# Kernel optimization log

Measured on AMD Instinct MI355X. Metric: run time of the kernel, lower is better.

Reference implementation:

```python
import jax, jax.numpy as jnp
import numpy as np

N_NODES = 100000
N_EDGES = 1600000
N_GRAPHS = 2000
IN_DIM = 37
HID = 128
OUT_CLS = 2


def _leconv(x, src, dst, w, W1, b1, W2, W3, b3):
    # PyG LEConv: out[i] = sum_j w_ij * (lin1(x)[i] - lin2(x)[j]) + lin3(x)[i]
    a = x @ W1 + b1          # [N, H]
    b = x @ W2               # [N, H] (lin2 has no bias)
    c = x @ W3 + b3          # [N, H]
    deg = jax.ops.segment_sum(w, dst, num_segments=N_NODES)              # [N]
    agg = jax.ops.segment_sum(w[:, None] * b[src], dst, num_segments=N_NODES)  # [N, H]
    return deg[:, None] * a - agg + c


def setup_inputs() -> dict:
    key = jax.random.key(0)
    ks = jax.random.split(key, 32)
    inp = {}
    inp["x"] = jax.random.normal(ks[0], (N_NODES, IN_DIM), dtype=jnp.float32)
    inp["edge_index"] = jax.random.randint(ks[1], (2, N_EDGES), 0, N_NODES, dtype=jnp.int64)
    inp["batch"] = jnp.sort(jax.random.randint(ks[2], (N_NODES,), 0, N_GRAPHS, dtype=jnp.int64))
    dims = [(IN_DIM, HID), (HID, HID), (HID, HID)]
    ki = 3
    for l, (di, do) in enumerate(dims):
        s = 1.0 / np.sqrt(di)
        inp[f"W1_{l}"] = jax.random.uniform(ks[ki + 0], (di, do), jnp.float32, -s, s)
        inp[f"b1_{l}"] = jax.random.uniform(ks[ki + 1], (do,), jnp.float32, -s, s)
        inp[f"W2_{l}"] = jax.random.uniform(ks[ki + 2], (di, do), jnp.float32, -s, s)
        inp[f"W3_{l}"] = jax.random.uniform(ks[ki + 3], (di, do), jnp.float32, -s, s)
        inp[f"b3_{l}"] = jax.random.uniform(ks[ki + 4], (do,), jnp.float32, -s, s)
        ki += 5
    sf = 1.0 / np.sqrt(HID)
    inp["Wf1"] = jax.random.uniform(ks[ki + 0], (HID, HID), jnp.float32, -sf, sf)
    inp["bf1"] = jax.random.uniform(ks[ki + 1], (HID,), jnp.float32, -sf, sf)
    inp["Wf2"] = jax.random.uniform(ks[ki + 2], (HID, OUT_CLS), jnp.float32, -sf, sf)
    inp["bf2"] = jax.random.uniform(ks[ki + 3], (OUT_CLS,), jnp.float32, -sf, sf)
    return inp


def reference(x, edge_index, batch,
              W1_0, b1_0, W2_0, W3_0, b3_0,
              W1_1, b1_1, W2_1, W3_1, b3_1,
              W1_2, b1_2, W2_2, W3_2, b3_2,
              Wf1, bf1, Wf2, bf2):
    src, dst = edge_index[0], edge_index[1]
    w = jnp.ones((edge_index.shape[1],), dtype=x.dtype)  # edge_weight = ones
    layers = [(W1_0, b1_0, W2_0, W3_0, b3_0),
              (W1_1, b1_1, W2_1, W3_1, b3_1),
              (W1_2, b1_2, W2_2, W3_2, b3_2)]
    h = x
    for (W1, b1, W2, W3, b3) in layers:
        h = jax.nn.relu(_leconv(h, src, dst, w, W1, b1, W2, W3, b3))
    # global mean pool per graph
    sums = jax.ops.segment_sum(h, batch, num_segments=N_GRAPHS)           # [G, H]
    cnt = jax.ops.segment_sum(jnp.ones((N_NODES,), h.dtype), batch, num_segments=N_GRAPHS)
    graph_x = sums / jnp.clip(cnt, 1.0)[:, None]
    # FFN head (Dropout is identity at inference)
    pred = jax.nn.relu(graph_x @ Wf1 + bf1) @ Wf2 + bf2                   # [G, 2]
    return pred
```

## Files before the change

### kernel.cpp

```cpp
#include <hip/hip_runtime.h>
#include <hip/hip_bf16.h>
#include <cstdint>

#define N_NODES 100000
#define N_EDGES 1600000
#define N_GRAPHS 2000
#define IN_DIM 37
#define HID 128

#define FILL_BLOCKS 6250
#define CONV_BLOCKS 6250
#define PACK_BLOCKS 480
#define GEMM_GRID   1563

typedef __attribute__((ext_vector_type(8))) short short8;
typedef __attribute__((ext_vector_type(4))) float f32x4;

static __device__ __forceinline__ short bf16_bits(float f) {
    __hip_bfloat16 h = __float2bfloat16(f);
    return *reinterpret_cast<short*>(&h);
}
static __device__ __forceinline__ float bf16_lo(uint32_t u) {
    uint32_t v = u << 16;
    return *reinterpret_cast<float*>(&v);
}
static __device__ __forceinline__ float bf16_hi(uint32_t u) {
    uint32_t v = u & 0xffff0000u;
    return *reinterpret_cast<float*>(&v);
}


struct PackArgs {
    const float* w[9];
    short* o[9];
};

__global__ __launch_bounds__(256) void fused_hist_conv_pack(const int* __restrict__ ei,
                                                            int* __restrict__ cnt,
                                                            int* __restrict__ rank,
                                                            const float* __restrict__ x,
                                                            short* __restrict__ Xb,
                                                            PackArgs pa) {
    const int b = blockIdx.x;
    const int tid = threadIdx.x;

    if (b < FILL_BLOCKS) {
        const int e = b * 256 + tid;
        const int d = ei[N_EDGES + e];
        rank[e] = atomicAdd(&cnt[d], 1);
        return;
    }
    if (b < FILL_BLOCKS + CONV_BLOCKS) {
        const int idx = (b - FILL_BLOCKS) * 256 + tid;
        const int n = idx >> 4, j = idx & 15;
        const int k0 = j * 4;
        short4 o;
        o.x = (k0 + 0 < IN_DIM) ? bf16_bits(x[(size_t)n * IN_DIM + k0 + 0]) : (short)0;
        o.y = (k0 + 1 < IN_DIM) ? bf16_bits(x[(size_t)n * IN_DIM + k0 + 1]) : (short)0;
        o.z = (k0 + 2 < IN_DIM) ? bf16_bits(x[(size_t)n * IN_DIM + k0 + 2]) : (short)0;
        o.w = (k0 + 3 < IN_DIM) ? bf16_bits(x[(size_t)n * IN_DIM + k0 + 3]) : (short)0;
        *(short4*)(Xb + (size_t)n * 64 + k0) = o;
        return;
    }
    int idx = (b - FILL_BLOCKS - CONV_BLOCKS) * 256 + tid;
    int m, r, kin;
    if (idx < 24576) { m = idx >> 13; r = idx & 8191; kin = IN_DIM; }
    else { int q = idx - 24576; m = 3 + (q >> 14); r = q & 16383; kin = HID; }
    const int i = r & 7, lane = (r >> 3) & 63, t = (r >> 9) & 7, kb = r >> 12;
    const int k = kb * 32 + (lane >> 4) * 8 + i;
    const int c = t * 16 + (lane & 15);
    float v = (k < kin) ? pa.w[m][(size_t)k * HID + c] : 0.f;
    pa.o[m][r] = bf16_bits(v);
}


__global__ __launch_bounds__(1024) void scan_blocks(const int* __restrict__ cnt,
                                                    int* __restrict__ partial,
                                                    int* __restrict__ bsum) {
    __shared__ int ws[16];
    const int tid = threadIdx.x, lane = tid & 63, wv = tid >> 6;
    const int i = blockIdx.x * 1024 + tid;
    int v0 = (i < N_NODES) ? cnt[i] : 0;
    int v = v0;
    #pragma unroll
    for (int off = 1; off < 64; off <<= 1) {
        int n = __shfl_up(v, off, 64);
        if (lane >= off) v += n;
    }
    if (lane == 63) ws[wv] = v;
    __syncthreads();
    int woff = 0, tot = 0;
    #pragma unroll
    for (int w = 0; w < 16; w++) {
        int s = ws[w];
        if (w < wv) woff += s;
        tot += s;
    }
    if (i < N_NODES) partial[i] = woff + v - v0;
    if (tid == 0) bsum[blockIdx.x] = tot;
}

__global__ __launch_bounds__(1024) void scan_finalize(const int* __restrict__ partial,
                                                      const int* __restrict__ bsum,
                                                      const int* __restrict__ cnt,
                                                      int* __restrict__ rowptr,
                                                      float* __restrict__ degf) {
    __shared__ int off_s;
    const int tid = threadIdx.x, b = blockIdx.x;
    if (tid < 64) {
        int acc = 0;
        for (int j = tid; j < b; j += 64) acc += bsum[j];
        #pragma unroll
        for (int off = 32; off; off >>= 1) acc += __shfl_down(acc, off, 64);
        if (tid == 0) off_s = acc;
    }
    __syncthreads();
    const int i = b * 1024 + tid;
    if (i < N_NODES) {
        rowptr[i] = off_s + partial[i];
        degf[i] = (float)cnt[i];
    }
    if (b == 0 && tid == 0) rowptr[N_NODES] = N_EDGES;
}


template <int K32>
static __device__ __forceinline__ void leconv_body(
    int blk,
    const short* __restrict__ Hb,
    const short* __restrict__ Wp1, const short* __restrict__ Wp2, const short* __restrict__ Wp3,
    const float* __restrict__ b1v, const float* __restrict__ b3v,
    const float* __restrict__ deg,
    short* __restrict__ Bb, float* __restrict__ OUT) {
    constexpr int K = K32 * 32;
    const int tid = threadIdx.x;
    const int wave = tid >> 6, lane = tid & 63;
    const int row_base = blk * 64 + wave * 16;
    const int r15 = lane & 15, kg = lane >> 4;

    int arow = row_base + r15;
    if (arow >= N_NODES) arow = N_NODES - 1;
    const short* aptr = Hb + (size_t)arow * K + kg * 8;

    f32x4 acc1[8], acc2[8], acc3[8];
    #pragma unroll
    for (int t = 0; t < 8; t++) {
        acc1[t] = (f32x4)0.f; acc2[t] = (f32x4)0.f; acc3[t] = (f32x4)0.f;
    }

    #pragma unroll
    for (int kb = 0; kb < K32; kb++) {
        short8 a = *(const short8*)(aptr + kb * 32);
        #pragma unroll
        for (int t = 0; t < 8; t++) {
            const int widx = (kb * 8 + t) * 512 + lane * 8;
            short8 w1 = *(const short8*)(Wp1 + widx);
            short8 w2 = *(const short8*)(Wp2 + widx);
            short8 w3 = *(const short8*)(Wp3 + widx);
            acc1[t] = __builtin_amdgcn_mfma_f32_16x16x32_bf16(a, w1, acc1[t], 0, 0, 0);
            acc2[t] = __builtin_amdgcn_mfma_f32_16x16x32_bf16(a, w2, acc2[t], 0, 0, 0);
            acc3[t] = __builtin_amdgcn_mfma_f32_16x16x32_bf16(a, w3, acc3[t], 0, 0, 0);
        }
    }

    int grow[4];
    bool ok[4];
    float dg[4];
    #pragma unroll
    for (int i = 0; i < 4; i++) {
        grow[i] = row_base + kg * 4 + i;
        ok[i] = grow[i] < N_NODES;
        dg[i] = ok[i] ? deg[grow[i]] : 0.f;
    }
    #pragma unroll
    for (int t = 0; t < 8; t++) {
        const int c = t * 16 + r15;
        const float bb1 = b1v[c], bb3 = b3v[c];
        #pragma unroll
        for (int i = 0; i < 4; i++) {
            if (ok[i]) {
                size_t o = (size_t)grow[i] * HID + c;
                OUT[o] = dg[i] * (acc1[t][i] + bb1) + acc3[t][i] + bb3;
                Bb[o] = bf16_bits(acc2[t][i]);
            }
        }
    }
}

template <int K32>
__global__ __launch_bounds__(256) void leconv_mfma(
    const short* __restrict__ Hb,
    const short* __restrict__ Wp1, const short* __restrict__ Wp2, const short* __restrict__ Wp3,
    const float* __restrict__ b1v, const float* __restrict__ b3v,
    const float* __restrict__ deg,
    short* __restrict__ Bb, float* __restrict__ OUT) {
    leconv_body<K32>(blockIdx.x, Hb, Wp1, Wp2, Wp3, b1v, b3v, deg, Bb, OUT);
}


__global__ __launch_bounds__(256) void fused_fill_gemm(
    const int* __restrict__ ei, const int* __restrict__ rank, const int* __restrict__ rowptr,
    int* __restrict__ col,
    const short* __restrict__ Xb,
    const short* __restrict__ Wp1, const short* __restrict__ Wp2, const short* __restrict__ Wp3,
    const float* __restrict__ b1v, const float* __restrict__ b3v,
    const float* __restrict__ deg,
    short* __restrict__ Bb, float* __restrict__ OUT) {
    const int b = blockIdx.x;
    if (b < FILL_BLOCKS) {
        const int e = b * 256 + threadIdx.x;
        const int s = ei[e];
        const int d = ei[N_EDGES + e];
        col[rowptr[d] + rank[e]] = s;
        return;
    }
    leconv_body<2>(b - FILL_BLOCKS, Xb, Wp1, Wp2, Wp3, b1v, b3v, deg, Bb, OUT);
}


__global__ __launch_bounds__(256) void gather_csr(const int* __restrict__ rowptr,
                                                  const int* __restrict__ col,
                                                  const short* __restrict__ Bb,
                                                  const float* __restrict__ OUT,
                                                  short* __restrict__ Hb) {
    const int wid = (blockIdx.x * 256 + threadIdx.x) >> 6;
    const int lane = threadIdx.x & 63;
    if (wid >= N_NODES) return;
    const int s = rowptr[wid], e = rowptr[wid + 1];
    float ax0 = 0.f, ay0 = 0.f, ax1 = 0.f, ay1 = 0.f;
    int t = s;
    for (; t + 4 <= e; t += 4) {
        const int c0 = col[t], c1 = col[t + 1], c2 = col[t + 2], c3 = col[t + 3];
        const uint32_t u0 = *(const uint32_t*)(Bb + (size_t)c0 * HID + lane * 2);
        const uint32_t u1 = *(const uint32_t*)(Bb + (size_t)c1 * HID + lane * 2);
        const uint32_t u2 = *(const uint32_t*)(Bb + (size_t)c2 * HID + lane * 2);
        const uint32_t u3 = *(const uint32_t*)(Bb + (size_t)c3 * HID + lane * 2);
        ax0 += bf16_lo(u0) + bf16_lo(u2);
        ay0 += bf16_hi(u0) + bf16_hi(u2);
        ax1 += bf16_lo(u1) + bf16_lo(u3);
        ay1 += bf16_hi(u1) + bf16_hi(u3);
    }
    for (; t < e; t++) {
        const int c0 = col[t];
        const uint32_t u0 = *(const uint32_t*)(Bb + (size_t)c0 * HID + lane * 2);
        ax0 += bf16_lo(u0);
        ay0 += bf16_hi(u0);
    }
    const float ax = ax0 + ax1, ay = ay0 + ay1;
    const float2 o = *(const float2*)(OUT + (size_t)wid * HID + lane * 2);
    const float ox = fmaxf(o.x - ax, 0.f);
    const float oy = fmaxf(o.y - ay, 0.f);
    const uint32_t r = ((uint32_t)(uint16_t)bf16_bits(oy) << 16) | (uint16_t)bf16_bits(ox);
    *(uint32_t*)(Hb + (size_t)wid * HID + lane * 2) = r;
}


__global__ __launch_bounds__(128) void pool_ffn_kernel(const short* __restrict__ H,
                                                       const int* __restrict__ batch,
                                                       const float* __restrict__ Wf1,
                                                       const float* __restrict__ bf1,
                                                       const float* __restrict__ Wf2,
                                                       const float* __restrict__ bf2,
                                                       float* __restrict__ out) {
    const int g = blockIdx.x;
    const int t = threadIdx.x;

    int lo = 0, hi = N_NODES;
    while (lo < hi) { int mid = (lo + hi) >> 1; if (batch[mid] < g) lo = mid + 1; else hi = mid; }
    const int s = lo;
    hi = N_NODES;
    while (lo < hi) { int mid = (lo + hi) >> 1; if (batch[mid] < g + 1) lo = mid + 1; else hi = mid; }
    const int e = lo;

    float sum = 0.f;
    for (int n = s; n < e; n++) {
        short b = H[(size_t)n * HID + t];
        sum += __bfloat162float(*(__hip_bfloat16*)&b);
    }
    const float cntf = (float)(e - s);
    const float gx = sum / fmaxf(cntf, 1.f);

    __shared__ float lds[HID];
    lds[t] = gx;
    __syncthreads();

    float hsum = bf1[t];
    #pragma unroll 8
    for (int k = 0; k < HID; k++) hsum = fmaf(lds[k], Wf1[k * HID + t], hsum);
    const float hr = fmaxf(hsum, 0.f);

    float p0 = hr * Wf2[t * 2 + 0];
    float p1 = hr * Wf2[t * 2 + 1];
    #pragma unroll
    for (int off = 32; off > 0; off >>= 1) {
        p0 += __shfl_down(p0, off, 64);
        p1 += __shfl_down(p1, off, 64);
    }
    __shared__ float red[4];
    if ((t & 63) == 0) {
        red[(t >> 6) * 2 + 0] = p0;
        red[(t >> 6) * 2 + 1] = p1;
    }
    __syncthreads();
    if (t == 0) {
        out[g * 2 + 0] = red[0] + red[2] + bf2[0];
        out[g * 2 + 1] = red[1] + red[3] + bf2[1];
    }
}


extern "C" void kernel_launch(void* const* d_in, const int* in_sizes, int n_in,
                              void* d_out, int out_size, void* d_ws, size_t ws_size,
                              hipStream_t stream) {
    (void)in_sizes; (void)n_in; (void)out_size; (void)ws_size;

    const float* x     = (const float*)d_in[0];
    const int*   ei    = (const int*)d_in[1];
    const int*   batch = (const int*)d_in[2];
    const float* W[9] = {
        (const float*)d_in[3],  (const float*)d_in[5],  (const float*)d_in[6],
        (const float*)d_in[8],  (const float*)d_in[10], (const float*)d_in[11],
        (const float*)d_in[13], (const float*)d_in[15], (const float*)d_in[16]};
    const float* b1_0 = (const float*)d_in[4];
    const float* b3_0 = (const float*)d_in[7];
    const float* b1_1 = (const float*)d_in[9];
    const float* b3_1 = (const float*)d_in[12];
    const float* b1_2 = (const float*)d_in[14];
    const float* b3_2 = (const float*)d_in[17];
    const float* Wf1  = (const float*)d_in[18];
    const float* bf1  = (const float*)d_in[19];
    const float* Wf2  = (const float*)d_in[20];
    const float* bf2  = (const float*)d_in[21];
    float* out = (float*)d_out;

    char* ws = (char*)d_ws;
    size_t off = 0;
    auto alloc = [&](size_t bytes) {
        void* p = ws + off;
        off += (bytes + 255) & ~(size_t)255;
        return p;
    };
    float* OUT    = (float*)alloc((size_t)N_NODES * HID * 4);
    short* Bb     = (short*)alloc((size_t)N_NODES * HID * 2);
    short* Hb     = (short*)alloc((size_t)N_NODES * HID * 2);
    short* Xb     = (short*)alloc((size_t)N_NODES * 64 * 2);
    float* degf   = (float*)alloc((size_t)N_NODES * 4);
    int*   rowptr = (int*)alloc((size_t)(N_NODES + 1) * 4);
    int*   cnt    = (int*)alloc((size_t)N_NODES * 4);
    int*   col    = (int*)alloc((size_t)N_EDGES * 4);
    int*   rank   = (int*)alloc((size_t)N_EDGES * 4);
    int*   partial= (int*)alloc((size_t)N_NODES * 4);
    int*   bsum   = (int*)alloc(1024);
    short* P[9];
    for (int m = 0; m < 9; m++) P[m] = (short*)alloc(16384 * 2);

    hipMemsetAsync(cnt, 0, (size_t)N_NODES * 4, stream);

    PackArgs pa;
    for (int m = 0; m < 9; m++) { pa.w[m] = W[m]; pa.o[m] = P[m]; }

    fused_hist_conv_pack<<<FILL_BLOCKS + CONV_BLOCKS + PACK_BLOCKS, 256, 0, stream>>>(
        ei, cnt, rank, x, Xb, pa);

    const int NSB = (N_NODES + 1023) / 1024;
    scan_blocks<<<NSB, 1024, 0, stream>>>(cnt, partial, bsum);
    scan_finalize<<<NSB, 1024, 0, stream>>>(partial, bsum, cnt, rowptr, degf);

    fused_fill_gemm<<<FILL_BLOCKS + GEMM_GRID, 256, 0, stream>>>(
        ei, rank, rowptr, col, Xb, P[0], P[1], P[2], b1_0, b3_0, degf, Bb, OUT);

    const int gather_grid = (N_NODES * 64 + 255) / 256;

    gather_csr<<<gather_grid, 256, 0, stream>>>(rowptr, col, Bb, OUT, Hb);
    leconv_mfma<4><<<GEMM_GRID, 256, 0, stream>>>(Hb, P[3], P[4], P[5], b1_1, b3_1, degf, Bb, OUT);
    gather_csr<<<gather_grid, 256, 0, stream>>>(rowptr, col, Bb, OUT, Hb);
    leconv_mfma<4><<<GEMM_GRID, 256, 0, stream>>>(Hb, P[6], P[7], P[8], b1_2, b3_2, degf, Bb, OUT);
    gather_csr<<<gather_grid, 256, 0, stream>>>(rowptr, col, Bb, OUT, Hb);
    pool_ffn_kernel<<<N_GRAPHS, 128, 0, stream>>>(Hb, batch, Wf1, bf1, Wf2, bf2, out);
}
```

Measured before the change: 518.4 us.

## Fuse CSR gather into following LEConv MFMA GEMM via LDS staging

```diff
diff --git a/kernel.cpp b/kernel.cpp
--- a/kernel.cpp
+++ b/kernel.cpp
@@ -185,16 +185,6 @@
             }
         }
     }
-}
-
-template <int K32>
-__global__ __launch_bounds__(256) void leconv_mfma(
-    const short* __restrict__ Hb,
-    const short* __restrict__ Wp1, const short* __restrict__ Wp2, const short* __restrict__ Wp3,
-    const float* __restrict__ b1v, const float* __restrict__ b3v,
-    const float* __restrict__ deg,
-    short* __restrict__ Bb, float* __restrict__ OUT) {
-    leconv_body<K32>(blockIdx.x, Hb, Wp1, Wp2, Wp3, b1v, b3v, deg, Bb, OUT);
 }
 
 
@@ -215,6 +205,98 @@
         return;
     }
     leconv_body<2>(b - FILL_BLOCKS, Xb, Wp1, Wp2, Wp3, b1v, b3v, deg, Bb, OUT);
+}
+
+
+__global__ __launch_bounds__(256) void gather_gemm(
+    const int* __restrict__ rowptr, const int* __restrict__ col,
+    const short* __restrict__ Bb_prev, const float* __restrict__ OUT_prev,
+    const short* __restrict__ Wp1, const short* __restrict__ Wp2, const short* __restrict__ Wp3,
+    const float* __restrict__ b1v, const float* __restrict__ b3v,
+    const float* __restrict__ deg,
+    short* __restrict__ Bb_out, float* __restrict__ OUT_out) {
+    __shared__ short hs[4][16][136];
+
+    const int tid = threadIdx.x;
+    const int wave = tid >> 6, lane = tid & 63;
+    const int row_base = blockIdx.x * 64 + wave * 16;
+
+    for (int r = 0; r < 16; r++) {
+        int node = row_base + r;
+        int nc = (node < N_NODES) ? node : N_NODES - 1;
+        const int s = rowptr[nc], e = rowptr[nc + 1];
+        float ax0 = 0.f, ay0 = 0.f, ax1 = 0.f, ay1 = 0.f;
+        int t = s;
+        for (; t + 4 <= e; t += 4) {
+            const int c0 = col[t], c1 = col[t + 1], c2 = col[t + 2], c3 = col[t + 3];
+            const uint32_t u0 = *(const uint32_t*)(Bb_prev + (size_t)c0 * HID + lane * 2);
+            const uint32_t u1 = *(const uint32_t*)(Bb_prev + (size_t)c1 * HID + lane * 2);
+            const uint32_t u2 = *(const uint32_t*)(Bb_prev + (size_t)c2 * HID + lane * 2);
+            const uint32_t u3 = *(const uint32_t*)(Bb_prev + (size_t)c3 * HID + lane * 2);
+            ax0 += bf16_lo(u0) + bf16_lo(u2);
+            ay0 += bf16_hi(u0) + bf16_hi(u2);
+            ax1 += bf16_lo(u1) + bf16_lo(u3);
+            ay1 += bf16_hi(u1) + bf16_hi(u3);
+        }
+        for (; t < e; t++) {
+            const int c0 = col[t];
+            const uint32_t u0 = *(const uint32_t*)(Bb_prev + (size_t)c0 * HID + lane * 2);
+            ax0 += bf16_lo(u0);
+            ay0 += bf16_hi(u0);
+        }
+        const float2 o = *(const float2*)(OUT_prev + (size_t)nc * HID + lane * 2);
+        const float ox = fmaxf(o.x - (ax0 + ax1), 0.f);
+        const float oy = fmaxf(o.y - (ay0 + ay1), 0.f);
+        const uint32_t pk = ((uint32_t)(uint16_t)bf16_bits(oy) << 16) | (uint16_t)bf16_bits(ox);
+        *(uint32_t*)&hs[wave][r][lane * 2] = pk;
+    }
+
+    const int r15 = lane & 15, kg = lane >> 4;
+    const short* aptr = &hs[wave][r15][kg * 8];
+
+    f32x4 acc1[8], acc2[8], acc3[8];
+    #pragma unroll
+    for (int t = 0; t < 8; t++) {
+        acc1[t] = (f32x4)0.f; acc2[t] = (f32x4)0.f; acc3[t] = (f32x4)0.f;
+    }
+
+    #pragma unroll
+    for (int kb = 0; kb < 4; kb++) {
+        short8 a = *(const short8*)(aptr + kb * 32);
+        #pragma unroll
+        for (int t = 0; t < 8; t++) {
+            const int widx = (kb * 8 + t) * 512 + lane * 8;
+            short8 w1 = *(const short8*)(Wp1 + widx);
+            short8 w2 = *(const short8*)(Wp2 + widx);
+            short8 w3 = *(const short8*)(Wp3 + widx);
+            acc1[t] = __builtin_amdgcn_mfma_f32_16x16x32_bf16(a, w1, acc1[t], 0, 0, 0);
+            acc2[t] = __builtin_amdgcn_mfma_f32_16x16x32_bf16(a, w2, acc2[t], 0, 0, 0);
+            acc3[t] = __builtin_amdgcn_mfma_f32_16x16x32_bf16(a, w3, acc3[t], 0, 0, 0);
+        }
+    }
+
+    int grow[4];
+    bool ok[4];
+    float dg[4];
+    #pragma unroll
+    for (int i = 0; i < 4; i++) {
+        grow[i] = row_base + kg * 4 + i;
+        ok[i] = grow[i] < N_NODES;
+        dg[i] = ok[i] ? deg[grow[i]] : 0.f;
+    }
+    #pragma unroll
+    for (int t = 0; t < 8; t++) {
+        const int c = t * 16 + r15;
+        const float bb1 = b1v[c], bb3 = b3v[c];
+        #pragma unroll
+        for (int i = 0; i < 4; i++) {
+            if (ok[i]) {
+                size_t o = (size_t)grow[i] * HID + c;
+                OUT_out[o] = dg[i] * (acc1[t][i] + bb1) + acc3[t][i] + bb3;
+                Bb_out[o] = bf16_bits(acc2[t][i]);
+            }
+        }
+    }
 }
 
 
@@ -340,8 +422,10 @@
         off += (bytes + 255) & ~(size_t)255;
         return p;
     };
-    float* OUT    = (float*)alloc((size_t)N_NODES * HID * 4);
-    short* Bb     = (short*)alloc((size_t)N_NODES * HID * 2);
+    float* OUT_A  = (float*)alloc((size_t)N_NODES * HID * 4);
+    float* OUT_B  = (float*)alloc((size_t)N_NODES * HID * 4);
+    short* Bb_A   = (short*)alloc((size_t)N_NODES * HID * 2);
+    short* Bb_B   = (short*)alloc((size_t)N_NODES * HID * 2);
     short* Hb     = (short*)alloc((size_t)N_NODES * HID * 2);
     short* Xb     = (short*)alloc((size_t)N_NODES * 64 * 2);
     float* degf   = (float*)alloc((size_t)N_NODES * 4);
@@ -367,14 +451,16 @@
     scan_finalize<<<NSB, 1024, 0, stream>>>(partial, bsum, cnt, rowptr, degf);
 
     fused_fill_gemm<<<FILL_BLOCKS + GEMM_GRID, 256, 0, stream>>>(
-        ei, rank, rowptr, col, Xb, P[0], P[1], P[2], b1_0, b3_0, degf, Bb, OUT);
+        ei, rank, rowptr, col, Xb, P[0], P[1], P[2], b1_0, b3_0, degf, Bb_A, OUT_A);
+
+    gather_gemm<<<GEMM_GRID, 256, 0, stream>>>(
+        rowptr, col, Bb_A, OUT_A, P[3], P[4], P[5], b1_1, b3_1, degf, Bb_B, OUT_B);
+
+    gather_gemm<<<GEMM_GRID, 256, 0, stream>>>(
+        rowptr, col, Bb_B, OUT_B, P[6], P[7], P[8], b1_2, b3_2, degf, Bb_A, OUT_A);
 
     const int gather_grid = (N_NODES * 64 + 255) / 256;
-
-    gather_csr<<<gather_grid, 256, 0, stream>>>(rowptr, col, Bb, OUT, Hb);
-    leconv_mfma<4><<<GEMM_GRID, 256, 0, stream>>>(Hb, P[3], P[4], P[5], b1_1, b3_1, degf, Bb, OUT);
-    gather_csr<<<gather_grid, 256, 0, stream>>>(rowptr, col, Bb, OUT, Hb);
-    leconv_mfma<4><<<GEMM_GRID, 256, 0, stream>>>(Hb, P[6], P[7], P[8], b1_2, b3_2, degf, Bb, OUT);
-    gather_csr<<<gather_grid, 256, 0, stream>>>(rowptr, col, Bb, OUT, Hb);
+    gather_csr<<<gather_grid, 256, 0, stream>>>(rowptr, col, Bb_A, OUT_A, Hb);
+
     pool_ffn_kernel<<<N_GRAPHS, 128, 0, stream>>>(Hb, batch, Wf1, bf1, Wf2, bf2, out);
 }
```

Result: slower. 777.8 us (+50.1%).

## Move layer-0 GEMM ahead of degree scan and store per-node outputs as bf16

Applied to the files above, without the earlier changes.

```diff
diff --git a/kernel.cpp b/kernel.cpp
--- a/kernel.cpp
+++ b/kernel.cpp
@@ -8,10 +8,10 @@
 #define IN_DIM 37
 #define HID 128
 
-#define FILL_BLOCKS 6250
-#define CONV_BLOCKS 6250
-#define PACK_BLOCKS 480
-#define GEMM_GRID   1563
+#define GEMM_GRID 1563
+#define HIST_BLOCKS 6250
+#define PACK67_BLOCKS 384
+#define PREPACK_BLOCKS 96
 
 typedef __attribute__((ext_vector_type(8))) short short8;
 typedef __attribute__((ext_vector_type(4))) float f32x4;
@@ -35,42 +35,104 @@
     short* o[9];
 };
 
-__global__ __launch_bounds__(256) void fused_hist_conv_pack(const int* __restrict__ ei,
-                                                            int* __restrict__ cnt,
-                                                            int* __restrict__ rank,
-                                                            const float* __restrict__ x,
-                                                            short* __restrict__ Xb,
-                                                            PackArgs pa) {
-    const int b = blockIdx.x;
-    const int tid = threadIdx.x;
-
-    if (b < FILL_BLOCKS) {
-        const int e = b * 256 + tid;
-        const int d = ei[N_EDGES + e];
-        rank[e] = atomicAdd(&cnt[d], 1);
-        return;
-    }
-    if (b < FILL_BLOCKS + CONV_BLOCKS) {
-        const int idx = (b - FILL_BLOCKS) * 256 + tid;
-        const int n = idx >> 4, j = idx & 15;
-        const int k0 = j * 4;
-        short4 o;
-        o.x = (k0 + 0 < IN_DIM) ? bf16_bits(x[(size_t)n * IN_DIM + k0 + 0]) : (short)0;
-        o.y = (k0 + 1 < IN_DIM) ? bf16_bits(x[(size_t)n * IN_DIM + k0 + 1]) : (short)0;
-        o.z = (k0 + 2 < IN_DIM) ? bf16_bits(x[(size_t)n * IN_DIM + k0 + 2]) : (short)0;
-        o.w = (k0 + 3 < IN_DIM) ? bf16_bits(x[(size_t)n * IN_DIM + k0 + 3]) : (short)0;
-        *(short4*)(Xb + (size_t)n * 64 + k0) = o;
-        return;
-    }
-    int idx = (b - FILL_BLOCKS - CONV_BLOCKS) * 256 + tid;
-    int m, r, kin;
-    if (idx < 24576) { m = idx >> 13; r = idx & 8191; kin = IN_DIM; }
-    else { int q = idx - 24576; m = 3 + (q >> 14); r = q & 16383; kin = HID; }
+static __device__ __forceinline__ void pack_one(const PackArgs& pa, int m, int r, int kin) {
     const int i = r & 7, lane = (r >> 3) & 63, t = (r >> 9) & 7, kb = r >> 12;
     const int k = kb * 32 + (lane >> 4) * 8 + i;
     const int c = t * 16 + (lane & 15);
     float v = (k < kin) ? pa.w[m][(size_t)k * HID + c] : 0.f;
     pa.o[m][r] = bf16_bits(v);
+}
+
+__global__ __launch_bounds__(256) void prepack_kernel(PackArgs pa) {
+    const int idx = blockIdx.x * 256 + threadIdx.x;
+    pack_one(pa, idx >> 13, idx & 8191, IN_DIM);
+}
+
+
+static __device__ __forceinline__ void gemm0_body(
+    int blk, const float* __restrict__ x,
+    const short* __restrict__ Wp1, const short* __restrict__ Wp2, const short* __restrict__ Wp3,
+    const float* __restrict__ b1v, const float* __restrict__ b3v,
+    short* __restrict__ D0, short* __restrict__ E0, short* __restrict__ Bb) {
+    const int tid = threadIdx.x;
+    const int wave = tid >> 6, lane = tid & 63;
+    const int row_base = blk * 64 + wave * 16;
+    const int r15 = lane & 15, kg = lane >> 4;
+    int arow = row_base + r15;
+    if (arow >= N_NODES) arow = N_NODES - 1;
+    const float* xr = x + (size_t)arow * IN_DIM;
+
+    f32x4 acc1[8], acc2[8], acc3[8];
+    #pragma unroll
+    for (int t = 0; t < 8; t++) {
+        acc1[t] = (f32x4)0.f; acc2[t] = (f32x4)0.f; acc3[t] = (f32x4)0.f;
+    }
+    #pragma unroll
+    for (int kb = 0; kb < 2; kb++) {
+        short8 av;
+        #pragma unroll
+        for (int i = 0; i < 8; i++) {
+            const int k = kb * 32 + kg * 8 + i;
+            av[i] = (k < IN_DIM) ? bf16_bits(xr[k]) : (short)0;
+        }
+        #pragma unroll
+        for (int t = 0; t < 8; t++) {
+            const int widx = (kb * 8 + t) * 512 + lane * 8;
+            short8 w1 = *(const short8*)(Wp1 + widx);
+            short8 w2 = *(const short8*)(Wp2 + widx);
+            short8 w3 = *(const short8*)(Wp3 + widx);
+            acc1[t] = __builtin_amdgcn_mfma_f32_16x16x32_bf16(av, w1, acc1[t], 0, 0, 0);
+            acc2[t] = __builtin_amdgcn_mfma_f32_16x16x32_bf16(av, w2, acc2[t], 0, 0, 0);
+            acc3[t] = __builtin_amdgcn_mfma_f32_16x16x32_bf16(av, w3, acc3[t], 0, 0, 0);
+        }
+    }
+    int grow[4]; bool ok[4];
+    #pragma unroll
+    for (int i = 0; i < 4; i++) {
+        grow[i] = row_base + kg * 4 + i;
+        ok[i] = grow[i] < N_NODES;
+    }
+    #pragma unroll
+    for (int t = 0; t < 8; t++) {
+        const int c = t * 16 + r15;
+        const float bb1 = b1v[c], bb3 = b3v[c];
+        #pragma unroll
+        for (int i = 0; i < 4; i++) {
+            if (ok[i]) {
+                size_t o = (size_t)grow[i] * HID + c;
+                D0[o] = bf16_bits(acc1[t][i] + bb1);
+                E0[o] = bf16_bits(acc3[t][i] + bb3);
+                Bb[o] = bf16_bits(acc2[t][i]);
+            }
+        }
+    }
+}
+
+
+struct P1Args {
+    const float* x;
+    const int* ei;
+    int* cnt; int* rank;
+    const short* Wp1; const short* Wp2; const short* Wp3;
+    const float* b1; const float* b3;
+    short* D0; short* E0; short* Bb;
+    PackArgs pa;
+};
+
+__global__ __launch_bounds__(256) void phase1_kernel(P1Args a) {
+    const int b = blockIdx.x;
+    if (b < GEMM_GRID) {
+        gemm0_body(b, a.x, a.Wp1, a.Wp2, a.Wp3, a.b1, a.b3, a.D0, a.E0, a.Bb);
+        return;
+    }
+    if (b < GEMM_GRID + HIST_BLOCKS) {
+        const int e = (b - GEMM_GRID) * 256 + threadIdx.x;
+        const int d = a.ei[N_EDGES + e];
+        a.rank[e] = atomicAdd(&a.cnt[d], 1);
+        return;
+    }
+    const int idx = (b - GEMM_GRID - HIST_BLOCKS) * 256 + threadIdx.x;
+    pack_one(a.pa, 3 + (idx >> 14), idx & 16383, HID);
 }
 
 
@@ -124,48 +186,118 @@
 }
 
 
-template <int K32>
-static __device__ __forceinline__ void leconv_body(
-    int blk,
+__global__ __launch_bounds__(256) void fill_kernel(const int* __restrict__ ei,
+                                                   const int* __restrict__ rank,
+                                                   const int* __restrict__ rowptr,
+                                                   int* __restrict__ col) {
+    const int e = blockIdx.x * 256 + threadIdx.x;
+    const int s = ei[e];
+    const int d = ei[N_EDGES + e];
+    col[rowptr[d] + rank[e]] = s;
+}
+
+
+static __device__ __forceinline__ void agg_edges(const int* __restrict__ col, int s, int e,
+                                                 const short* __restrict__ Bb, int lane2,
+                                                 float& AX, float& AY) {
+    float ax0 = 0.f, ay0 = 0.f, ax1 = 0.f, ay1 = 0.f;
+    int t = s;
+    for (; t < e && (t & 3); t++) {
+        const uint32_t u = *(const uint32_t*)(Bb + (size_t)col[t] * HID + lane2);
+        ax0 += bf16_lo(u); ay0 += bf16_hi(u);
+    }
+    for (; t + 4 <= e; t += 4) {
+        const int4 c4 = *(const int4*)(col + t);
+        const uint32_t u0 = *(const uint32_t*)(Bb + (size_t)c4.x * HID + lane2);
+        const uint32_t u1 = *(const uint32_t*)(Bb + (size_t)c4.y * HID + lane2);
+        const uint32_t u2 = *(const uint32_t*)(Bb + (size_t)c4.z * HID + lane2);
+        const uint32_t u3 = *(const uint32_t*)(Bb + (size_t)c4.w * HID + lane2);
+        ax0 += bf16_lo(u0) + bf16_lo(u2);
+        ay0 += bf16_hi(u0) + bf16_hi(u2);
+        ax1 += bf16_lo(u1) + bf16_lo(u3);
+        ay1 += bf16_hi(u1) + bf16_hi(u3);
+    }
+    for (; t < e; t++) {
+        const uint32_t u = *(const uint32_t*)(Bb + (size_t)col[t] * HID + lane2);
+        ax0 += bf16_lo(u); ay0 += bf16_hi(u);
+    }
+    AX = ax0 + ax1; AY = ay0 + ay1;
+}
+
+__global__ __launch_bounds__(256) void gather0_kernel(const int* __restrict__ rowptr,
+                                                      const int* __restrict__ col,
+                                                      const short* __restrict__ Bb,
+                                                      const short* __restrict__ D0,
+                                                      const short* __restrict__ E0,
+                                                      short* __restrict__ Hb) {
+    const int wid = (blockIdx.x * 256 + threadIdx.x) >> 6;
+    const int lane2 = (threadIdx.x & 63) * 2;
+    if (wid >= N_NODES) return;
+    const int s = rowptr[wid], e = rowptr[wid + 1];
+    float ax, ay;
+    agg_edges(col, s, e, Bb, lane2, ax, ay);
+    const float dg = (float)(e - s);
+    const uint32_t ud = *(const uint32_t*)(D0 + (size_t)wid * HID + lane2);
+    const uint32_t ue = *(const uint32_t*)(E0 + (size_t)wid * HID + lane2);
+    const float ox = fmaxf(fmaf(dg, bf16_lo(ud), bf16_lo(ue)) - ax, 0.f);
+    const float oy = fmaxf(fmaf(dg, bf16_hi(ud), bf16_hi(ue)) - ay, 0.f);
+    *(uint32_t*)(Hb + (size_t)wid * HID + lane2) =
+        ((uint32_t)(uint16_t)bf16_bits(oy) << 16) | (uint16_t)bf16_bits(ox);
+}
+
+__global__ __launch_bounds__(256) void gatherL_kernel(const int* __restrict__ rowptr,
+                                                      const int* __restrict__ col,
+                                                      const short* __restrict__ Bb,
+                                                      const short* __restrict__ OUTb,
+                                                      short* __restrict__ Hb) {
+    const int wid = (blockIdx.x * 256 + threadIdx.x) >> 6;
+    const int lane2 = (threadIdx.x & 63) * 2;
+    if (wid >= N_NODES) return;
+    const int s = rowptr[wid], e = rowptr[wid + 1];
+    float ax, ay;
+    agg_edges(col, s, e, Bb, lane2, ax, ay);
+    const uint32_t uo = *(const uint32_t*)(OUTb + (size_t)wid * HID + lane2);
+    const float ox = fmaxf(bf16_lo(uo) - ax, 0.f);
+    const float oy = fmaxf(bf16_hi(uo) - ay, 0.f);
+    *(uint32_t*)(Hb + (size_t)wid * HID + lane2) =
+        ((uint32_t)(uint16_t)bf16_bits(oy) << 16) | (uint16_t)bf16_bits(ox);
+}
+
+
+__global__ __launch_bounds__(256) void leconv_mfma(
     const short* __restrict__ Hb,
     const short* __restrict__ Wp1, const short* __restrict__ Wp2, const short* __restrict__ Wp3,
     const float* __restrict__ b1v, const float* __restrict__ b3v,
     const float* __restrict__ deg,
-    short* __restrict__ Bb, float* __restrict__ OUT) {
-    constexpr int K = K32 * 32;
+    short* __restrict__ Bb, short* __restrict__ OUTb) {
     const int tid = threadIdx.x;
     const int wave = tid >> 6, lane = tid & 63;
-    const int row_base = blk * 64 + wave * 16;
+    const int row_base = blockIdx.x * 64 + wave * 16;
     const int r15 = lane & 15, kg = lane >> 4;
-
     int arow = row_base + r15;
     if (arow >= N_NODES) arow = N_NODES - 1;
-    const short* aptr = Hb + (size_t)arow * K + kg * 8;
+    const short* aptr = Hb + (size_t)arow * HID + kg * 8;
 
     f32x4 acc1[8], acc2[8], acc3[8];
     #pragma unroll
     for (int t = 0; t < 8; t++) {
         acc1[t] = (f32x4)0.f; acc2[t] = (f32x4)0.f; acc3[t] = (f32x4)0.f;
     }
-
-    #pragma unroll
-    for (int kb = 0; kb < K32; kb++) {
-        short8 a = *(const short8*)(aptr + kb * 32);
+    #pragma unroll
+    for (int kb = 0; kb < 4; kb++) {
+        short8 av = *(const short8*)(aptr + kb * 32);
         #pragma unroll
         for (int t = 0; t < 8; t++) {
             const int widx = (kb * 8 + t) * 512 + lane * 8;
             short8 w1 = *(const short8*)(Wp1 + widx);
             short8 w2 = *(const short8*)(Wp2 + widx);
             short8 w3 = *(const short8*)(Wp3 + widx);
-            acc1[t] = __builtin_amdgcn_mfma_f32_16x16x32_bf16(a, w1, acc1[t], 0, 0, 0);
-            acc2[t] = __builtin_amdgcn_mfma_f32_16x16x32_bf16(a, w2, acc2[t], 0, 0, 0);
-            acc3[t] = __builtin_amdgcn_mfma_f32_16x16x32_bf16(a, w3, acc3[t], 0, 0, 0);
+            acc1[t] = __builtin_amdgcn_mfma_f32_16x16x32_bf16(av, w1, acc1[t], 0, 0, 0);
+            acc2[t] = __builtin_amdgcn_mfma_f32_16x16x32_bf16(av, w2, acc2[t], 0, 0, 0);
+            acc3[t] = __builtin_amdgcn_mfma_f32_16x16x32_bf16(av, w3, acc3[t], 0, 0, 0);
         }
     }
-
-    int grow[4];
-    bool ok[4];
-    float dg[4];
+    int grow[4]; bool ok[4]; float dg[4];
     #pragma unroll
     for (int i = 0; i < 4; i++) {
         grow[i] = row_base + kg * 4 + i;
@@ -180,78 +312,11 @@
         for (int i = 0; i < 4; i++) {
             if (ok[i]) {
                 size_t o = (size_t)grow[i] * HID + c;
-                OUT[o] = dg[i] * (acc1[t][i] + bb1) + acc3[t][i] + bb3;
+                OUTb[o] = bf16_bits(dg[i] * (acc1[t][i] + bb1) + acc3[t][i] + bb3);
                 Bb[o] = bf16_bits(acc2[t][i]);
             }
         }
     }
-}
-
-template <int K32>
-__global__ __launch_bounds__(256) void leconv_mfma(
-    const short* __restrict__ Hb,
-    const short* __restrict__ Wp1, const short* __restrict__ Wp2, const short* __restrict__ Wp3,
-    const float* __restrict__ b1v, const float* __restrict__ b3v,
-    const float* __restrict__ deg,
-    short* __restrict__ Bb, float* __restrict__ OUT) {
-    leconv_body<K32>(blockIdx.x, Hb, Wp1, Wp2, Wp3, b1v, b3v, deg, Bb, OUT);
-}
-
-
-__global__ __launch_bounds__(256) void fused_fill_gemm(
-    const int* __restrict__ ei, const int* __restrict__ rank, const int* __restrict__ rowptr,
-    int* __restrict__ col,
-    const short* __restrict__ Xb,
-    const short* __restrict__ Wp1, const short* __restrict__ Wp2, const short* __restrict__ Wp3,
-    const float* __restrict__ b1v, const float* __restrict__ b3v,
-    const float* __restrict__ deg,
-    short* __restrict__ Bb, float* __restrict__ OUT) {
-    const int b = blockIdx.x;
-    if (b < FILL_BLOCKS) {
-        const int e = b * 256 + threadIdx.x;
-        const int s = ei[e];
-        const int d = ei[N_EDGES + e];
-        col[rowptr[d] + rank[e]] = s;
-        return;
-    }
-    leconv_body<2>(b - FILL_BLOCKS, Xb, Wp1, Wp2, Wp3, b1v, b3v, deg, Bb, OUT);
-}
-
-
-__global__ __launch_bounds__(256) void gather_csr(const int* __restrict__ rowptr,
-                                                  const int* __restrict__ col,
-                                                  const short* __restrict__ Bb,
-                                                  const float* __restrict__ OUT,
-                                                  short* __restrict__ Hb) {
-    const int wid = (blockIdx.x * 256 + threadIdx.x) >> 6;
-    const int lane = threadIdx.x & 63;
-    if (wid >= N_NODES) return;
-    const int s = rowptr[wid], e = rowptr[wid + 1];
-    float ax0 = 0.f, ay0 = 0.f, ax1 = 0.f, ay1 = 0.f;
-    int t = s;
-    for (; t + 4 <= e; t += 4) {
-        const int c0 = col[t], c1 = col[t + 1], c2 = col[t + 2], c3 = col[t + 3];
-        const uint32_t u0 = *(const uint32_t*)(Bb + (size_t)c0 * HID + lane * 2);
-        const uint32_t u1 = *(const uint32_t*)(Bb + (size_t)c1 * HID + lane * 2);
-        const uint32_t u2 = *(const uint32_t*)(Bb + (size_t)c2 * HID + lane * 2);
-        const uint32_t u3 = *(const uint32_t*)(Bb + (size_t)c3 * HID + lane * 2);
-        ax0 += bf16_lo(u0) + bf16_lo(u2);
-        ay0 += bf16_hi(u0) + bf16_hi(u2);
-        ax1 += bf16_lo(u1) + bf16_lo(u3);
-        ay1 += bf16_hi(u1) + bf16_hi(u3);
-    }
-    for (; t < e; t++) {
-        const int c0 = col[t];
-        const uint32_t u0 = *(const uint32_t*)(Bb + (size_t)c0 * HID + lane * 2);
-        ax0 += bf16_lo(u0);
-        ay0 += bf16_hi(u0);
-    }
-    const float ax = ax0 + ax1, ay = ay0 + ay1;
-    const float2 o = *(const float2*)(OUT + (size_t)wid * HID + lane * 2);
-    const float ox = fmaxf(o.x - ax, 0.f);
-    const float oy = fmaxf(o.y - ay, 0.f);
-    const uint32_t r = ((uint32_t)(uint16_t)bf16_bits(oy) << 16) | (uint16_t)bf16_bits(ox);
-    *(uint32_t*)(Hb + (size_t)wid * HID + lane * 2) = r;
 }
 
 
@@ -340,10 +405,11 @@
         off += (bytes + 255) & ~(size_t)255;
         return p;
     };
-    float* OUT    = (float*)alloc((size_t)N_NODES * HID * 4);
-    short* Bb     = (short*)alloc((size_t)N_NODES * HID * 2);
+    short* D0     = (short*)alloc((size_t)N_NODES * HID * 2);
+    short* E0     = (short*)alloc((size_t)N_NODES * HID * 2);
+    short* Bb_A   = (short*)alloc((size_t)N_NODES * HID * 2);
+    short* Bb_B   = (short*)alloc((size_t)N_NODES * HID * 2);
     short* Hb     = (short*)alloc((size_t)N_NODES * HID * 2);
-    short* Xb     = (short*)alloc((size_t)N_NODES * 64 * 2);
     float* degf   = (float*)alloc((size_t)N_NODES * 4);
     int*   rowptr = (int*)alloc((size_t)(N_NODES + 1) * 4);
     int*   cnt    = (int*)alloc((size_t)N_NODES * 4);
@@ -359,22 +425,24 @@
     PackArgs pa;
     for (int m = 0; m < 9; m++) { pa.w[m] = W[m]; pa.o[m] = P[m]; }
 
-    fused_hist_conv_pack<<<FILL_BLOCKS + CONV_BLOCKS + PACK_BLOCKS, 256, 0, stream>>>(
-        ei, cnt, rank, x, Xb, pa);
+    prepack_kernel<<<PREPACK_BLOCKS, 256, 0, stream>>>(pa);
+
+    P1Args p1{ x, ei, cnt, rank, P[0], P[1], P[2], b1_0, b3_0, D0, E0, Bb_A, pa };
+    phase1_kernel<<<GEMM_GRID + HIST_BLOCKS + PACK67_BLOCKS, 256, 0, stream>>>(p1);
 
     const int NSB = (N_NODES + 1023) / 1024;
     scan_blocks<<<NSB, 1024, 0, stream>>>(cnt, partial, bsum);
     scan_finalize<<<NSB, 1024, 0, stream>>>(partial, bsum, cnt, rowptr, degf);
 
-    fused_fill_gemm<<<FILL_BLOCKS + GEMM_GRID, 256, 0, stream>>>(
-        ei, rank, rowptr, col, Xb, P[0], P[1], P[2], b1_0, b3_0, degf, Bb, OUT);
+    fill_kernel<<<HIST_BLOCKS, 256, 0, stream>>>(ei, rank, rowptr, col);
 
     const int gather_grid = (N_NODES * 64 + 255) / 256;
 
-    gather_csr<<<gather_grid, 256, 0, stream>>>(rowptr, col, Bb, OUT, Hb);
-    leconv_mfma<4><<<GEMM_GRID, 256, 0, stream>>>(Hb, P[3], P[4], P[5], b1_1, b3_1, degf, Bb, OUT);
-    gather_csr<<<gather_grid, 256, 0, stream>>>(rowptr, col, Bb, OUT, Hb);
-    leconv_mfma<4><<<GEMM_GRID, 256, 0, stream>>>(Hb, P[6], P[7], P[8], b1_2, b3_2, degf, Bb, OUT);
-    gather_csr<<<gather_grid, 256, 0, stream>>>(rowptr, col, Bb, OUT, Hb);
+    gather0_kernel<<<gather_grid, 256, 0, stream>>>(rowptr, col, Bb_A, D0, E0, Hb);
+    leconv_mfma<<<GEMM_GRID, 256, 0, stream>>>(Hb, P[3], P[4], P[5], b1_1, b3_1, degf, Bb_B, E0);
+    gatherL_kernel<<<gather_grid, 256, 0, stream>>>(rowptr, col, Bb_B, E0, Hb);
+    leconv_mfma<<<GEMM_GRID, 256, 0, stream>>>(Hb, P[6], P[7], P[8], b1_2, b3_2, degf, Bb_A, D0);
+    gatherL_kernel<<<gather_grid, 256, 0, stream>>>(rowptr, col, Bb_A, D0, Hb);
+
     pool_ffn_kernel<<<N_GRAPHS, 128, 0, stream>>>(Hb, batch, Wf1, bf1, Wf2, bf2, out);
 }
```

Result: no change. 526.5 us (+1.6%).
